# Kernel tuning notes

Measured on AMD Instinct MI355X. Metric: run time of the kernel, lower is better.

Reference implementation:

```python
import jax, jax.numpy as jnp
import numpy as np

DROPOUT_P = 0.5
INV_SCALE = 1.0
_DROP_KEY = jax.random.key(42)


def setup_inputs() -> dict:
    key = jax.random.key(0)
    kq, kk, kv = jax.random.split(key, 3)
    B, H, S, D = 4, 16, 2048, 64
    return {
        "query": jax.random.normal(kq, (B, H, S, D), dtype=jnp.float32),
        "key": jax.random.normal(kk, (B, H, S, D), dtype=jnp.float32),
        "value": jax.random.normal(kv, (B, H, S, D), dtype=jnp.float32),
    }


def reference(query, key, value):
    # qk = Q @ K^T, scaled, softmax over last axis
    qk = jnp.einsum("bhqd,bhkd->bhqk", query, key) / INV_SCALE
    p = jax.nn.softmax(qk, axis=-1)
    # inverted dropout with a fixed RNG key (deterministic reference)
    keep = jax.random.bernoulli(_DROP_KEY, 1.0 - DROPOUT_P, p.shape)
    p = jnp.where(keep, p / (1.0 - DROPOUT_P), 0.0)
    # attention output: P @ V
    return jnp.einsum("bhqk,bhkd->bhqd", p, value)
```

## Files before the change

### kernel.cpp

```cpp
#include <hip/hip_runtime.h>


#define S_LEN 2048
#define D_DIM 64
#define KT    32
#define QT    16
#define NWAVE 4
#define KSTR  72
#define VROW  66
#define PSTR  40

typedef short  short8  __attribute__((ext_vector_type(8)));
typedef float  floatx4 __attribute__((ext_vector_type(4)));
typedef unsigned uint2v __attribute__((ext_vector_type(2)));

#define TF_R2(sh) \
  "v_add_u32 %1, %1, %0\n\t" \
  "v_add_u32 %3, %3, %2\n\t" \
  "v_alignbit_b32 %0, %0, %0, " #sh "\n\t" \
  "v_alignbit_b32 %2, %2, %2, " #sh "\n\t" \
  "v_xor_b32 %0, %0, %1\n\t" \
  "v_xor_b32 %2, %2, %3\n\t"

__device__ __forceinline__ void tf2(unsigned i0, unsigned i1,
                                    unsigned& w0, unsigned& w1) {
  unsigned a0, a1;
  asm(
    "v_add_u32 %0, 42, %4\n\t"
    "v_add_u32 %2, 42, %5\n\t"
    "v_mov_b32 %1, %0\n\t"
    "v_mov_b32 %3, %2\n\t"
    "v_alignbit_b32 %0, %0, %0, 19\n\t"
    "v_alignbit_b32 %2, %2, %2, 19\n\t"
    "v_xor_b32 %0, %0, %1\n\t"
    "v_xor_b32 %2, %2, %3\n\t"
    TF_R2(17) TF_R2(6) TF_R2(26)
    "v_add_u32 %1, 42, %1\n\t"
    "v_add_u32 %3, 42, %3\n\t"
    "v_add_u32 %0, 0x1bd11bf1, %0\n\t"
    "v_add_u32 %2, 0x1bd11bf1, %2\n\t"
    TF_R2(15) TF_R2(3) TF_R2(16) TF_R2(8)
    "v_add_u32 %1, 0x1bd11bf0, %1\n\t"
    "v_add_u32 %3, 0x1bd11bf0, %3\n\t"
    "v_add_u32 %0, 2, %0\n\t"
    "v_add_u32 %2, 2, %2\n\t"
    TF_R2(19) TF_R2(17) TF_R2(6) TF_R2(26)
    "v_add_u32 %0, 45, %0\n\t"
    "v_add_u32 %2, 45, %2\n\t"
    TF_R2(15) TF_R2(3) TF_R2(16) TF_R2(8)
    "v_add_u32 %1, 42, %1\n\t"
    "v_add_u32 %3, 42, %3\n\t"
    "v_add_u32 %0, 0x1bd11bf4, %0\n\t"
    "v_add_u32 %2, 0x1bd11bf4, %2\n\t"
    TF_R2(19) TF_R2(17) TF_R2(6) TF_R2(26)
    "v_add_u32 %1, 0x1bd11bf0, %1\n\t"
    "v_add_u32 %3, 0x1bd11bf0, %3\n\t"
    "v_add_u32 %0, 5, %0\n\t"
    "v_add_u32 %2, 5, %2\n\t"
    "v_xor_b32 %0, %0, %1\n\t"
    "v_xor_b32 %2, %2, %3"
    : "=&v"(w0), "=&v"(a0), "=&v"(w1), "=&v"(a1)
    : "v"(i0), "v"(i1));
}

__device__ __forceinline__ void split_bf16(float x, unsigned short& h, unsigned short& l) {
  unsigned u = __float_as_uint(x);
  h = (unsigned short)(u >> 16);
  float r = x - __uint_as_float(u & 0xFFFF0000u);
  l = (unsigned short)(__float_as_uint(r) >> 16);
}

#define MFMA(a, b, c) __builtin_amdgcn_mfma_f32_16x16x32_bf16((a), (b), (c), 0, 0, 0)

__global__ __launch_bounds__(256) void prep_k(
    const float* __restrict__ Kg, unsigned short* __restrict__ KHg,
    unsigned short* __restrict__ KLg) {
  unsigned t  = blockIdx.x * 256u + threadIdx.x;
  unsigned i4 = t * 4u;
  floatx4 kv = *(const floatx4*)(Kg + i4);
  unsigned short h0, h1, h2, h3, l0, l1, l2, l3;
  split_bf16(kv[0], h0, l0); split_bf16(kv[1], h1, l1);
  split_bf16(kv[2], h2, l2); split_bf16(kv[3], h3, l3);
  uint2v hh, ll;
  hh[0] = (unsigned)h0 | ((unsigned)h1 << 16);
  hh[1] = (unsigned)h2 | ((unsigned)h3 << 16);
  ll[0] = (unsigned)l0 | ((unsigned)l1 << 16);
  ll[1] = (unsigned)l2 | ((unsigned)l3 << 16);
  *(uint2v*)(KHg + i4) = hh;
  *(uint2v*)(KLg + i4) = ll;
}

__global__ __launch_bounds__(256) void prep_vt(
    const float* __restrict__ Vg, unsigned short* __restrict__ VTg) {
  __shared__ unsigned short T[D_DIM][40];
  const int bh   = blockIdx.x >> 6;
  const int tile = blockIdx.x & 63;
  const int tid  = threadIdx.x;
  const int row  = tid >> 3;
  const int c8   = (tid & 7) * 8;
  const float* vp = Vg + (size_t)bh * S_LEN * D_DIM + (size_t)(tile * 32 + row) * D_DIM + c8;
  floatx4 v0 = *(const floatx4*)vp;
  floatx4 v1 = *(const floatx4*)(vp + 4);
#pragma unroll
  for (int e = 0; e < 4; ++e) {
    T[c8 + e][row]     = (unsigned short)(__float_as_uint(v0[e]) >> 16);
    T[c8 + 4 + e][row] = (unsigned short)(__float_as_uint(v1[e]) >> 16);
  }
  __syncthreads();
  const int col = tid >> 2;
  const int r0  = (tid & 3) * 8;
  short8 out = *(const short8*)&T[col][r0];
  *(short8*)(VTg + ((size_t)blockIdx.x * D_DIM) * 32 + (size_t)tid * 8) = out;
}

__global__ __launch_bounds__(256, 4) void attn_v13(
    const float* __restrict__ Qg, float* __restrict__ Og,
    const unsigned short* __restrict__ KHg,
    const unsigned short* __restrict__ KLg,
    const unsigned short* __restrict__ VTg) {

  __shared__ __attribute__((aligned(16))) unsigned short Ph[NWAVE][QT * PSTR];

  const int tid  = threadIdx.x;
  const int wave = tid >> 6;
  const int lane = tid & 63;
  const int m16  = lane & 15;
  const int quad = lane >> 4;

  const int bh    = blockIdx.x >> 5;
  const int qtile = blockIdx.x & 31;
  const int q0    = qtile * (QT * NWAVE) + wave * QT;
  const size_t head_off = (size_t)bh * S_LEN * D_DIM;

  short8 qh[2], ql[2];
#pragma unroll
  for (int kc = 0; kc < 2; ++kc) {
    const float* qp = Qg + head_off + (size_t)(q0 + m16) * D_DIM + kc * 32 + quad * 8;
    floatx4 f0 = *(const floatx4*)qp;
    floatx4 f1 = *(const floatx4*)(qp + 4);
#pragma unroll
    for (int e = 0; e < 4; ++e) {
      unsigned short h, l;
      split_bf16(f0[e], h, l);
      qh[kc][e] = (short)h;  ql[kc][e] = (short)l;
      split_bf16(f1[e], h, l);
      qh[kc][4 + e] = (short)h;  ql[kc][4 + e] = (short)l;
    }
  }

  floatx4 o_acc[4];
#pragma unroll
  for (int n = 0; n < 4; ++n) o_acc[n] = (floatx4){0.f, 0.f, 0.f, 0.f};
  float lsum[4];
#pragma unroll
  for (int r = 0; r < 4; ++r) lsum[r] = 0.f;

  const unsigned ibase0 =
      ((unsigned)(bh * S_LEN + q0 + quad * 4)) * (unsigned)S_LEN + (unsigned)m16;

  const unsigned short* khp = KHg + head_off + (size_t)(m16 * D_DIM + quad * 8);
  const unsigned short* klp = KLg + head_off + (size_t)(m16 * D_DIM + quad * 8);
  const unsigned short* vtp = VTg + head_off + (size_t)(m16 * 32 + quad * 8);

  unsigned short*       p_wr = &Ph[wave][(quad * 4) * PSTR + m16];
  const unsigned short* p_rd = &Ph[wave][m16 * PSTR + quad * 8];

  for (int kb = 0; kb < S_LEN; kb += KT) {
    const unsigned short* kh_i = khp + (size_t)kb * D_DIM;
    const unsigned short* kl_i = klp + (size_t)kb * D_DIM;
    const unsigned short* vt_i = vtp + (size_t)(kb >> 5) * (D_DIM * 32);
    short8 kfh[2][2], kfl[2][2], vf[4];
#pragma unroll
    for (int nb = 0; nb < 2; ++nb)
#pragma unroll
      for (int kc = 0; kc < 2; ++kc) {
        kfh[nb][kc] = *(const short8*)(kh_i + nb * 16 * D_DIM + kc * 32);
        kfl[nb][kc] = *(const short8*)(kl_i + nb * 16 * D_DIM + kc * 32);
      }
#pragma unroll
    for (int n = 0; n < 4; ++n)
      vf[n] = *(const short8*)(vt_i + n * 16 * 32);

    unsigned w[8];
#pragma unroll
    for (int r = 0; r < 4; ++r) {
      unsigned i0 = ibase0 + (unsigned)kb + (unsigned)(r * S_LEN);
      tf2(i0, i0 + 16u, w[r * 2], w[r * 2 + 1]);
    }

    floatx4 sc[2];
#pragma unroll
    for (int nb = 0; nb < 2; ++nb) {
      floatx4 acc = (floatx4){0.f, 0.f, 0.f, 0.f};
#pragma unroll
      for (int kc = 0; kc < 2; ++kc) {
        acc = MFMA(qh[kc], kfh[nb][kc], acc);
        acc = MFMA(qh[kc], kfl[nb][kc], acc);
        acc = MFMA(ql[kc], kfh[nb][kc], acc);
      }
      sc[nb] = acc;
    }

#pragma unroll
    for (int r = 0; r < 4; ++r)
#pragma unroll
      for (int nb = 0; nb < 2; ++nb) {
        float pe = __expf(sc[nb][r]);
        lsum[r] += pe;
        unsigned hbits = __float_as_uint(pe) >> 16;
        hbits = ((int)w[r * 2 + nb] < 0) ? 0u : hbits;
        p_wr[r * PSTR + nb * 16] = (unsigned short)hbits;
      }

    short8 pa = *(const short8*)p_rd;
#pragma unroll
    for (int n = 0; n < 4; ++n)
      o_acc[n] = MFMA(pa, vf[n], o_acc[n]);
  }

#pragma unroll
  for (int off = 8; off >= 1; off >>= 1)
#pragma unroll
    for (int r = 0; r < 4; ++r)
      lsum[r] += __shfl_xor(lsum[r], off, 64);

#pragma unroll
  for (int r = 0; r < 4; ++r) {
    float scale = 2.0f / lsum[r];
#pragma unroll
    for (int n = 0; n < 4; ++n) {
      Og[head_off + (size_t)(q0 + quad * 4 + r) * D_DIM + n * 16 + m16] =
          o_acc[n][r] * scale;
    }
  }
}

__global__ __launch_bounds__(256, 6) void attn_mono(
    const float* __restrict__ Qg, const float* __restrict__ Kg,
    const float* __restrict__ Vg, float* __restrict__ Og) {

  __shared__ __attribute__((aligned(16))) unsigned short Kh[KT * KSTR];
  __shared__ __attribute__((aligned(16))) unsigned short Kl[KT * KSTR];
  __shared__ __attribute__((aligned(16))) unsigned short Vs[KT * VROW];
  __shared__ __attribute__((aligned(16))) unsigned short Ph[NWAVE][QT * PSTR];

  const int tid  = threadIdx.x;
  const int wave = tid >> 6;
  const int lane = tid & 63;
  const int m16  = lane & 15;
  const int quad = lane >> 4;

  const int bh    = blockIdx.x >> 5;
  const int qtile = blockIdx.x & 31;
  const int q0    = qtile * (QT * NWAVE) + wave * QT;
  const size_t head_off = (size_t)bh * S_LEN * D_DIM;

  short8 qh[2], ql[2];
#pragma unroll
  for (int kc = 0; kc < 2; ++kc) {
    const float* qp = Qg + head_off + (size_t)(q0 + m16) * D_DIM + kc * 32 + quad * 8;
    floatx4 f0 = *(const floatx4*)qp;
    floatx4 f1 = *(const floatx4*)(qp + 4);
#pragma unroll
    for (int e = 0; e < 4; ++e) {
      unsigned short h, l;
      split_bf16(f0[e], h, l);
      qh[kc][e] = (short)h;  ql[kc][e] = (short)l;
      split_bf16(f1[e], h, l);
      qh[kc][4 + e] = (short)h;  ql[kc][4 + e] = (short)l;
    }
  }

  floatx4 o_acc[4];
#pragma unroll
  for (int n = 0; n < 4; ++n) o_acc[n] = (floatx4){0.f, 0.f, 0.f, 0.f};
  float lsum[4];
#pragma unroll
  for (int r = 0; r < 4; ++r) lsum[r] = 0.f;

  const unsigned ibase0 =
      ((unsigned)(bh * S_LEN + q0 + quad * 4)) * (unsigned)S_LEN + (unsigned)m16;

  for (int kb = 0; kb < S_LEN; kb += KT) {
    __syncthreads();
    for (int f = tid; f < KT * (D_DIM / 4); f += 256) {
      int row = f >> 4;
      int c4  = (f & 15) << 2;
      size_t goff = head_off + (size_t)(kb + row) * D_DIM + c4;
      floatx4 kv = *(const floatx4*)(Kg + goff);
      floatx4 vv = *(const floatx4*)(Vg + goff);
      unsigned short h0, h1, h2, h3, l0, l1, l2, l3;
      split_bf16(kv[0], h0, l0); split_bf16(kv[1], h1, l1);
      split_bf16(kv[2], h2, l2); split_bf16(kv[3], h3, l3);
      int kidx = row * KSTR + c4;
      *(unsigned*)&Kh[kidx]     = (unsigned)h0 | ((unsigned)h1 << 16);
      *(unsigned*)&Kh[kidx + 2] = (unsigned)h2 | ((unsigned)h3 << 16);
      *(unsigned*)&Kl[kidx]     = (unsigned)l0 | ((unsigned)l1 << 16);
      *(unsigned*)&Kl[kidx + 2] = (unsigned)l2 | ((unsigned)l3 << 16);
      unsigned v01 = (__float_as_uint(vv[0]) >> 16) |
                     (__float_as_uint(vv[1]) & 0xFFFF0000u);
      unsigned v23 = (__float_as_uint(vv[2]) >> 16) |
                     (__float_as_uint(vv[3]) & 0xFFFF0000u);
      int vidx = row * VROW + c4;
      *(unsigned*)&Vs[vidx]     = v01;
      *(unsigned*)&Vs[vidx + 2] = v23;
    }
    __syncthreads();

    floatx4 sc[2];
#pragma unroll
    for (int nb = 0; nb < 2; ++nb) {
      floatx4 acc = (floatx4){0.f, 0.f, 0.f, 0.f};
#pragma unroll
      for (int kc = 0; kc < 2; ++kc) {
        int bidx = (nb * 16 + m16) * KSTR + kc * 32 + quad * 8;
        short8 kbh = *(const short8*)&Kh[bidx];
        short8 kbl = *(const short8*)&Kl[bidx];
        acc = MFMA(qh[kc], kbh, acc);
        acc = MFMA(qh[kc], kbl, acc);
        acc = MFMA(ql[kc], kbh, acc);
      }
      sc[nb] = acc;
    }

#pragma unroll
    for (int r = 0; r < 4; ++r) {
      unsigned i0 = ibase0 + (unsigned)kb + (unsigned)(r * S_LEN);
      unsigned w0, w1;
      tf2(i0, i0 + 16u, w0, w1);
#pragma unroll
      for (int nb = 0; nb < 2; ++nb) {
        float pe = __expf(sc[nb][r]);
        lsum[r] += pe;
        unsigned hbits = __float_as_uint(pe) >> 16;
        unsigned w = nb ? w1 : w0;
        hbits = ((int)w < 0) ? 0u : hbits;
        Ph[wave][(quad * 4 + r) * PSTR + nb * 16 + m16] = (unsigned short)hbits;
      }
    }

    short8 pa = *(const short8*)&Ph[wave][m16 * PSTR + quad * 8];
#pragma unroll
    for (int n = 0; n < 4; ++n) {
      short8 vb;
#pragma unroll
      for (int j = 0; j < 8; ++j)
        vb[j] = (short)Vs[(quad * 8 + j) * VROW + n * 16 + m16];
      o_acc[n] = MFMA(pa, vb, o_acc[n]);
    }
  }

#pragma unroll
  for (int off = 8; off >= 1; off >>= 1)
#pragma unroll
    for (int r = 0; r < 4; ++r)
      lsum[r] += __shfl_xor(lsum[r], off, 64);

#pragma unroll
  for (int r = 0; r < 4; ++r) {
    float scale = 2.0f / lsum[r];
#pragma unroll
    for (int n = 0; n < 4; ++n) {
      Og[head_off + (size_t)(q0 + quad * 4 + r) * D_DIM + n * 16 + m16] =
          o_acc[n][r] * scale;
    }
  }
}

extern "C" void kernel_launch(void* const* d_in, const int* in_sizes, int n_in,
                              void* d_out, int out_size, void* d_ws, size_t ws_size,
                              hipStream_t stream) {
  (void)in_sizes; (void)n_in; (void)out_size;
  const float* Q = (const float*)d_in[0];
  const float* K = (const float*)d_in[1];
  const float* V = (const float*)d_in[2];
  float* O = (float*)d_out;

  const size_t KELTS = (size_t)64 * S_LEN * D_DIM;
  const size_t NEED  = 3 * KELTS * sizeof(unsigned short);
  if (d_ws != nullptr && ws_size >= NEED) {
    unsigned short* KH = (unsigned short*)d_ws;
    unsigned short* KL = KH + KELTS;
    unsigned short* VT = KL + KELTS;
    hipLaunchKernelGGL(prep_k, dim3((unsigned)(KELTS / 4 / 256)), dim3(256),
                       0, stream, K, KH, KL);
    hipLaunchKernelGGL(prep_vt, dim3(64 * 64), dim3(256), 0, stream, V, VT);
    hipLaunchKernelGGL(attn_v13, dim3(2048), dim3(256), 0, stream, Q, O, KH, KL, VT);
  } else {
    hipLaunchKernelGGL(attn_mono, dim3(2048), dim3(256), 0, stream, Q, K, V, O);
  }
}
```

Before: 744.6 us.

## Merge prep kernels and software-pipeline P@V with double-buffered P tile

Fuses the K split and V transpose prep kernels into one launch, which removes a kernel launch and its gap. The attention loop is restructured so the P@V MFMAs for the previous key block run while the QK^T and exp/dropout work for the current block proceeds. The P tile in LDS is double-buffered and the V fragments are carried across iterations to hide LDS latency. This costs more registers and doubles the shared memory for P, which could lower occupancy. The __syncthreads in the V branch of the merged prep kernel is safe because the branch is uniform per block.

```diff
diff --git a/kernel.cpp b/kernel.cpp
--- a/kernel.cpp
+++ b/kernel.cpp
@@ -72,54 +72,56 @@
 
 #define MFMA(a, b, c) __builtin_amdgcn_mfma_f32_16x16x32_bf16((a), (b), (c), 0, 0, 0)
 
-__global__ __launch_bounds__(256) void prep_k(
-    const float* __restrict__ Kg, unsigned short* __restrict__ KHg,
-    unsigned short* __restrict__ KLg) {
-  unsigned t  = blockIdx.x * 256u + threadIdx.x;
-  unsigned i4 = t * 4u;
-  floatx4 kv = *(const floatx4*)(Kg + i4);
-  unsigned short h0, h1, h2, h3, l0, l1, l2, l3;
-  split_bf16(kv[0], h0, l0); split_bf16(kv[1], h1, l1);
-  split_bf16(kv[2], h2, l2); split_bf16(kv[3], h3, l3);
-  uint2v hh, ll;
-  hh[0] = (unsigned)h0 | ((unsigned)h1 << 16);
-  hh[1] = (unsigned)h2 | ((unsigned)h3 << 16);
-  ll[0] = (unsigned)l0 | ((unsigned)l1 << 16);
-  ll[1] = (unsigned)l2 | ((unsigned)l3 << 16);
-  *(uint2v*)(KHg + i4) = hh;
-  *(uint2v*)(KLg + i4) = ll;
-}
-
-__global__ __launch_bounds__(256) void prep_vt(
-    const float* __restrict__ Vg, unsigned short* __restrict__ VTg) {
+__global__ __launch_bounds__(256) void prep_all(
+    const float* __restrict__ Kg, const float* __restrict__ Vg,
+    unsigned short* __restrict__ KHg, unsigned short* __restrict__ KLg,
+    unsigned short* __restrict__ VTg) {
   __shared__ unsigned short T[D_DIM][40];
-  const int bh   = blockIdx.x >> 6;
-  const int tile = blockIdx.x & 63;
-  const int tid  = threadIdx.x;
-  const int row  = tid >> 3;
-  const int c8   = (tid & 7) * 8;
-  const float* vp = Vg + (size_t)bh * S_LEN * D_DIM + (size_t)(tile * 32 + row) * D_DIM + c8;
-  floatx4 v0 = *(const floatx4*)vp;
-  floatx4 v1 = *(const floatx4*)(vp + 4);
-#pragma unroll
-  for (int e = 0; e < 4; ++e) {
-    T[c8 + e][row]     = (unsigned short)(__float_as_uint(v0[e]) >> 16);
-    T[c8 + 4 + e][row] = (unsigned short)(__float_as_uint(v1[e]) >> 16);
-  }
-  __syncthreads();
-  const int col = tid >> 2;
-  const int r0  = (tid & 3) * 8;
-  short8 out = *(const short8*)&T[col][r0];
-  *(short8*)(VTg + ((size_t)blockIdx.x * D_DIM) * 32 + (size_t)tid * 8) = out;
-}
-
-__global__ __launch_bounds__(256, 4) void attn_v13(
+  if (blockIdx.x < 8192) {
+    unsigned t  = blockIdx.x * 256u + threadIdx.x;
+    unsigned i4 = t * 4u;
+    floatx4 kv = *(const floatx4*)(Kg + i4);
+    unsigned short h0, h1, h2, h3, l0, l1, l2, l3;
+    split_bf16(kv[0], h0, l0); split_bf16(kv[1], h1, l1);
+    split_bf16(kv[2], h2, l2); split_bf16(kv[3], h3, l3);
+    uint2v hh, ll;
+    hh[0] = (unsigned)h0 | ((unsigned)h1 << 16);
+    hh[1] = (unsigned)h2 | ((unsigned)h3 << 16);
+    ll[0] = (unsigned)l0 | ((unsigned)l1 << 16);
+    ll[1] = (unsigned)l2 | ((unsigned)l3 << 16);
+    *(uint2v*)(KHg + i4) = hh;
+    *(uint2v*)(KLg + i4) = ll;
+  } else {
+    const int bid  = blockIdx.x - 8192;
+    const int bh   = bid >> 6;
+    const int tile = bid & 63;
+    const int tid  = threadIdx.x;
+    const int row  = tid >> 3;
+    const int c8   = (tid & 7) * 8;
+    const float* vp = Vg + (size_t)bh * S_LEN * D_DIM +
+                      (size_t)(tile * 32 + row) * D_DIM + c8;
+    floatx4 v0 = *(const floatx4*)vp;
+    floatx4 v1 = *(const floatx4*)(vp + 4);
+#pragma unroll
+    for (int e = 0; e < 4; ++e) {
+      T[c8 + e][row]     = (unsigned short)(__float_as_uint(v0[e]) >> 16);
+      T[c8 + 4 + e][row] = (unsigned short)(__float_as_uint(v1[e]) >> 16);
+    }
+    __syncthreads();
+    const int col = tid >> 2;
+    const int r0  = (tid & 3) * 8;
+    short8 out = *(const short8*)&T[col][r0];
+    *(short8*)(VTg + ((size_t)bid * D_DIM) * 32 + (size_t)tid * 8) = out;
+  }
+}
+
+__global__ __launch_bounds__(256, 4) void attn_v14(
     const float* __restrict__ Qg, float* __restrict__ Og,
     const unsigned short* __restrict__ KHg,
     const unsigned short* __restrict__ KLg,
     const unsigned short* __restrict__ VTg) {
 
-  __shared__ __attribute__((aligned(16))) unsigned short Ph[NWAVE][QT * PSTR];
+  __shared__ __attribute__((aligned(16))) unsigned short Ph[2][NWAVE][QT * PSTR];
 
   const int tid  = threadIdx.x;
   const int wave = tid >> 6;
@@ -162,29 +164,30 @@
   const unsigned short* klp = KLg + head_off + (size_t)(m16 * D_DIM + quad * 8);
   const unsigned short* vtp = VTg + head_off + (size_t)(m16 * 32 + quad * 8);
 
-  unsigned short*       p_wr = &Ph[wave][(quad * 4) * PSTR + m16];
-  const unsigned short* p_rd = &Ph[wave][m16 * PSTR + quad * 8];
-
-  for (int kb = 0; kb < S_LEN; kb += KT) {
-    const unsigned short* kh_i = khp + (size_t)kb * D_DIM;
-    const unsigned short* kl_i = klp + (size_t)kb * D_DIM;
-    const unsigned short* vt_i = vtp + (size_t)(kb >> 5) * (D_DIM * 32);
-    short8 kfh[2][2], kfl[2][2], vf[4];
+  unsigned short*       p_wr0 = &Ph[0][wave][(quad * 4) * PSTR + m16];
+  const unsigned short* p_rd0 = &Ph[0][wave][m16 * PSTR + quad * 8];
+  const int PBUF = NWAVE * QT * PSTR;
+
+  short8 vf_prev[4];
+  int cur = 0;
+
+  {
+    short8 kfh[2][2], kfl[2][2];
 #pragma unroll
     for (int nb = 0; nb < 2; ++nb)
 #pragma unroll
       for (int kc = 0; kc < 2; ++kc) {
-        kfh[nb][kc] = *(const short8*)(kh_i + nb * 16 * D_DIM + kc * 32);
-        kfl[nb][kc] = *(const short8*)(kl_i + nb * 16 * D_DIM + kc * 32);
+        kfh[nb][kc] = *(const short8*)(khp + nb * 16 * D_DIM + kc * 32);
+        kfl[nb][kc] = *(const short8*)(klp + nb * 16 * D_DIM + kc * 32);
       }
 #pragma unroll
     for (int n = 0; n < 4; ++n)
-      vf[n] = *(const short8*)(vt_i + n * 16 * 32);
+      vf_prev[n] = *(const short8*)(vtp + n * 16 * 32);
 
     unsigned w[8];
 #pragma unroll
     for (int r = 0; r < 4; ++r) {
-      unsigned i0 = ibase0 + (unsigned)kb + (unsigned)(r * S_LEN);
+      unsigned i0 = ibase0 + (unsigned)(r * S_LEN);
       tf2(i0, i0 + 16u, w[r * 2], w[r * 2 + 1]);
     }
 
@@ -209,13 +212,72 @@
         lsum[r] += pe;
         unsigned hbits = __float_as_uint(pe) >> 16;
         hbits = ((int)w[r * 2 + nb] < 0) ? 0u : hbits;
-        p_wr[r * PSTR + nb * 16] = (unsigned short)hbits;
-      }
-
-    short8 pa = *(const short8*)p_rd;
+        p_wr0[r * PSTR + nb * 16] = (unsigned short)hbits;
+      }
+  }
+
+  for (int kb = KT; kb < S_LEN; kb += KT) {
+    const unsigned short* kh_i = khp + (size_t)kb * D_DIM;
+    const unsigned short* kl_i = klp + (size_t)kb * D_DIM;
+    const unsigned short* vt_i = vtp + (size_t)(kb >> 5) * (D_DIM * 32);
+    short8 kfh[2][2], kfl[2][2], vf[4];
+#pragma unroll
+    for (int nb = 0; nb < 2; ++nb)
+#pragma unroll
+      for (int kc = 0; kc < 2; ++kc) {
+        kfh[nb][kc] = *(const short8*)(kh_i + nb * 16 * D_DIM + kc * 32);
+        kfl[nb][kc] = *(const short8*)(kl_i + nb * 16 * D_DIM + kc * 32);
+      }
 #pragma unroll
     for (int n = 0; n < 4; ++n)
-      o_acc[n] = MFMA(pa, vf[n], o_acc[n]);
+      vf[n] = *(const short8*)(vt_i + n * 16 * 32);
+
+    short8 pa = *(const short8*)(p_rd0 + cur * PBUF);
+#pragma unroll
+    for (int n = 0; n < 4; ++n)
+      o_acc[n] = MFMA(pa, vf_prev[n], o_acc[n]);
+
+    unsigned w[8];
+#pragma unroll
+    for (int r = 0; r < 4; ++r) {
+      unsigned i0 = ibase0 + (unsigned)kb + (unsigned)(r * S_LEN);
+      tf2(i0, i0 + 16u, w[r * 2], w[r * 2 + 1]);
+    }
+
+    floatx4 sc[2];
+#pragma unroll
+    for (int nb = 0; nb < 2; ++nb) {
+      floatx4 acc = (floatx4){0.f, 0.f, 0.f, 0.f};
+#pragma unroll
+      for (int kc = 0; kc < 2; ++kc) {
+        acc = MFMA(qh[kc], kfh[nb][kc], acc);
+        acc = MFMA(qh[kc], kfl[nb][kc], acc);
+        acc = MFMA(ql[kc], kfh[nb][kc], acc);
+      }
+      sc[nb] = acc;
+    }
+
+#pragma unroll
+    for (int r = 0; r < 4; ++r)
+#pragma unroll
+      for (int nb = 0; nb < 2; ++nb) {
+        float pe = __expf(sc[nb][r]);
+        lsum[r] += pe;
+        unsigned hbits = __float_as_uint(pe) >> 16;
+        hbits = ((int)w[r * 2 + nb] < 0) ? 0u : hbits;
+        p_wr0[(cur ^ 1) * PBUF + r * PSTR + nb * 16] = (unsigned short)hbits;
+      }
+
+#pragma unroll
+    for (int n = 0; n < 4; ++n) vf_prev[n] = vf[n];
+    cur ^= 1;
+  }
+
+  {
+    short8 pa = *(const short8*)(p_rd0 + cur * PBUF);
+#pragma unroll
+    for (int n = 0; n < 4; ++n)
+      o_acc[n] = MFMA(pa, vf_prev[n], o_acc[n]);
   }
 
 #pragma unroll
@@ -242,7 +304,7 @@
   __shared__ __attribute__((aligned(16))) unsigned short Kh[KT * KSTR];
   __shared__ __attribute__((aligned(16))) unsigned short Kl[KT * KSTR];
   __shared__ __attribute__((aligned(16))) unsigned short Vs[KT * VROW];
-  __shared__ __attribute__((aligned(16))) unsigned short Ph[NWAVE][QT * PSTR];
+  __shared__ __attribute__((aligned(16))) unsigned short Ps[NWAVE][QT * PSTR];
 
   const int tid  = threadIdx.x;
   const int wave = tid >> 6;
@@ -335,11 +397,11 @@
         unsigned hbits = __float_as_uint(pe) >> 16;
         unsigned w = nb ? w1 : w0;
         hbits = ((int)w < 0) ? 0u : hbits;
-        Ph[wave][(quad * 4 + r) * PSTR + nb * 16 + m16] = (unsigned short)hbits;
-      }
-    }
-
-    short8 pa = *(const short8*)&Ph[wave][m16 * PSTR + quad * 8];
+        Ps[wave][(quad * 4 + r) * PSTR + nb * 16 + m16] = (unsigned short)hbits;
+      }
+    }
+
+    short8 pa = *(const short8*)&Ps[wave][m16 * PSTR + quad * 8];
 #pragma unroll
     for (int n = 0; n < 4; ++n) {
       short8 vb;
@@ -382,10 +444,9 @@
     unsigned short* KH = (unsigned short*)d_ws;
     unsigned short* KL = KH + KELTS;
     unsigned short* VT = KL + KELTS;
-    hipLaunchKernelGGL(prep_k, dim3((unsigned)(KELTS / 4 / 256)), dim3(256),
-                       0, stream, K, KH, KL);
-    hipLaunchKernelGGL(prep_vt, dim3(64 * 64), dim3(256), 0, stream, V, VT);
-    hipLaunchKernelGGL(attn_v13, dim3(2048), dim3(256), 0, stream, Q, O, KH, KL, VT);
+    hipLaunchKernelGGL(prep_all, dim3(8192 + 4096), dim3(256), 0, stream,
+                       K, V, KH, KL, VT);
+    hipLaunchKernelGGL(attn_v14, dim3(2048), dim3(256), 0, stream, Q, O, KH, KL, VT);
   } else {
     hipLaunchKernelGGL(attn_mono, dim3(2048), dim3(256), 0, stream, Q, K, V, O);
   }
```

Result: no change. 743.8 us (-0.1%).
